# Performance work log

Measured on AMD Instinct MI355X. Metric: run time of the kernel, lower is better.

## Reference

```python
import jax, jax.numpy as jnp
import numpy as np

D_MODEL = 1024
NUM_HEADS = 16
D_K = D_MODEL // NUM_HEADS
NEG_INF = -1e9


def setup_inputs() -> dict:
    key = jax.random.key(0)
    ks = jax.random.split(key, 12)
    B, N_IMG, L_Q = 32, 576, 256
    img = jax.random.normal(ks[0], (B, N_IMG, D_MODEL), dtype=jnp.float32)
    que = jax.random.normal(ks[1], (B, L_Q, D_MODEL), dtype=jnp.float32)
    mask_img = jax.random.randint(ks[2], (B, N_IMG), 0, 2, dtype=jnp.int32)
    mask_que = jax.random.randint(ks[3], (B, L_Q), 0, 2, dtype=jnp.int32)
    s = 0.02  # init scale keeps scores in a sane range
    Wi = jax.random.normal(ks[4], (3, D_MODEL, D_MODEL), dtype=jnp.float32) * s
    bi = jax.random.normal(ks[5], (3, D_MODEL), dtype=jnp.float32) * s
    Wq = jax.random.normal(ks[6], (3, D_MODEL, D_MODEL), dtype=jnp.float32) * s
    bq = jax.random.normal(ks[7], (3, D_MODEL), dtype=jnp.float32) * s
    Wp = jax.random.normal(ks[8], (2, D_MODEL, D_MODEL), dtype=jnp.float32) * s
    bp = jax.random.normal(ks[9], (2, D_MODEL), dtype=jnp.float32) * s
    return {"img": img, "que": que, "Wi": Wi, "bi": bi, "Wq": Wq, "bq": bq,
            "Wp": Wp, "bp": bp, "mask_img": mask_img, "mask_que": mask_que}


def _proj_heads(x, W, b):
    # torch Linear: x @ W.T + b, then [B, L, H, d_k] -> [B, H, L, d_k]
    B, L, _ = x.shape
    out = jnp.einsum("bld,ed->ble", x, W) + b
    return out.reshape(B, L, NUM_HEADS, D_K).transpose(0, 2, 1, 3)


def _attention(q, k, v, mask_key):
    # q: [B,H,Lq,dk], k/v: [B,H,Lk,dk], mask_key: [B,Lk] (0 = masked)
    scores = jnp.einsum("bhqd,bhkd->bhqk", q, k) / jnp.sqrt(jnp.asarray(D_K, q.dtype))
    scores = jnp.where(mask_key[:, None, None, :] == 0, NEG_INF, scores)
    p = jax.nn.softmax(scores, axis=-1)
    attn = jnp.einsum("bhqk,bhkd->bhqd", p, v)
    B, H, Lq, dk = attn.shape
    return attn.transpose(0, 2, 1, 3).reshape(B, Lq, H * dk)


def reference(img, que, Wi, bi, Wq, bq, Wp, bp, mask_img, mask_que):
    iq = _proj_heads(img, Wi[0], bi[0])
    ik = _proj_heads(img, Wi[1], bi[1])
    iv = _proj_heads(img, Wi[2], bi[2])
    qq = _proj_heads(que, Wq[0], bq[0])
    qk = _proj_heads(que, Wq[1], bq[1])
    qv = _proj_heads(que, Wq[2], bq[2])
    q2i = _attention(iq, qk, qv, mask_que)  # [B, N_img, d_model]
    i2q = _attention(qq, ik, iv, mask_img)  # [B, L_q, d_model]
    out0 = jnp.einsum("bld,ed->ble", q2i, Wp[0]) + bp[0]
    out1 = jnp.einsum("bld,ed->ble", i2q, Wp[1]) + bp[1]
    return (out0, out1)
```

## Files before the change

kernel.cpp:

```cpp
#include <hip/hip_runtime.h>


typedef __bf16 bf16;
typedef __attribute__((ext_vector_type(8))) __bf16 bf16x8;
typedef __attribute__((ext_vector_type(4))) __bf16 bf16x4;
typedef __attribute__((ext_vector_type(2))) __bf16 bf16x2;
typedef __attribute__((ext_vector_type(4))) float f32x4;

__device__ __forceinline__ void g2lds16(const void* g, void* l) {
  __builtin_amdgcn_global_load_lds((const __attribute__((address_space(1))) void*)g,
                                   (__attribute__((address_space(3))) void*)l,
                                   16, 0, 0);
}

__global__ void cvt_bf16_multi(const float* s0, bf16* d0, int n0,
                               const float* s1, bf16* d1, int n1,
                               const float* s2, bf16* d2, int n2,
                               const float* s3, bf16* d3, int n3,
                               const float* s4, bf16* d4, int n4c) {
  const int total = n0 + n1 + n2 + n3 + n4c;
  const int stride = gridDim.x * blockDim.x;
  for (int i = blockIdx.x * blockDim.x + threadIdx.x; i < total; i += stride) {
    int j = i;
    const float* s; bf16* d;
    if (j < n0) { s = s0; d = d0; }
    else { j -= n0;
      if (j < n1) { s = s1; d = d1; }
      else { j -= n1;
        if (j < n2) { s = s2; d = d2; }
        else { j -= n2;
          if (j < n3) { s = s3; d = d3; }
          else { j -= n3; s = s4; d = d4; }
        }
      }
    }
    const float4 v = ((const float4*)s)[j];
    bf16x4 o = {(bf16)v.x, (bf16)v.y, (bf16)v.z, (bf16)v.w};
    ((bf16x4*)d)[j] = o;
  }
}

template <int MODE>
__global__ __launch_bounds__(512, 2)
void gemm_bt(const bf16* __restrict__ A, const bf16* __restrict__ Bw,
             const float* __restrict__ bias, void* __restrict__ outp, int Lrow) {
  __shared__ alignas(16) bf16 As[3][256 * 64];
  __shared__ alignas(16) bf16 Bs[3][128 * 64];
  const int tid = threadIdx.x;
  const int w = tid >> 6, lane = tid & 63;
  const int lr = lane & 15, quad = lane >> 4;
  const int i_q4 = quad * 4;
  const int mBase = blockIdx.y * 256, nBase = blockIdx.x * 128;
  const int wr = (w >> 1) * 64, wc = (w & 1) * 64;

  const int swl = (((lane & 7) ^ ((lane >> 3) & 7)) * 8);
  const bf16* Ab = A + (size_t)(mBase + (lane >> 3)) * 1024 + swl;
  const bf16* Bb = Bw + (size_t)(nBase + (lane >> 3)) * 1024 + swl;

  auto STAGE = [&](int kt, int s) {
    const int k0 = kt * 64;
#pragma unroll
    for (int c = 0; c < 4; ++c) {
      const int r = w * 32 + c * 8;
      g2lds16(Ab + (size_t)r * 1024 + k0, &As[s][r * 64]);
    }
#pragma unroll
    for (int c = 0; c < 2; ++c) {
      const int r = w * 16 + c * 8;
      g2lds16(Bb + (size_t)r * 1024 + k0, &Bs[s][r * 64]);
    }
  };

  f32x4 acc[4][4] = {};

  STAGE(0, 0);
  STAGE(1, 1);
  asm volatile("s_waitcnt vmcnt(6)" ::: "memory");
  __builtin_amdgcn_s_barrier();

  int s0 = 0;
  for (int t = 0; t < 16; ++t) {
    const int s2 = (s0 >= 1) ? s0 - 1 : s0 + 2;
    if (t + 2 < 16) STAGE(t + 2, s2);
    bf16x8 a[2][4], b[2][4];
#pragma unroll
    for (int ks = 0; ks < 2; ++ks) {
      const int sOff = ((quad | (ks << 2)) ^ (lr & 7)) * 8;
      const bf16* Ar = &As[s0][(wr + lr) * 64 + sOff];
      const bf16* Br = &Bs[s0][(wc + lr) * 64 + sOff];
#pragma unroll
      for (int i = 0; i < 4; ++i) a[ks][i] = *(const bf16x8*)(Ar + i * 1024);
#pragma unroll
      for (int j = 0; j < 4; ++j) b[ks][j] = *(const bf16x8*)(Br + j * 1024);
    }
    __builtin_amdgcn_s_setprio(1);
#pragma unroll
    for (int ks = 0; ks < 2; ++ks)
#pragma unroll
      for (int i = 0; i < 4; ++i)
#pragma unroll
        for (int j = 0; j < 4; ++j)
          acc[i][j] = __builtin_amdgcn_mfma_f32_16x16x32_bf16(a[ks][i], b[ks][j], acc[i][j], 0, 0, 0);
    __builtin_amdgcn_s_setprio(0);
    if (t < 14) {
      asm volatile("s_waitcnt vmcnt(6)" ::: "memory");
      __builtin_amdgcn_s_barrier();
    } else if (t == 14) {
      asm volatile("s_waitcnt vmcnt(0)" ::: "memory");
      __builtin_amdgcn_s_barrier();
    }
    s0 = (s0 < 2) ? s0 + 1 : 0;
  }

  if constexpr (MODE == 1) {
    float* out = (float*)outp;
#pragma unroll
    for (int j = 0; j < 4; ++j) {
      const int e = nBase + wc + j * 16 + lr;
      const float bv = bias[e];
#pragma unroll
      for (int i = 0; i < 4; ++i) {
        const int mb = mBase + wr + i * 16 + i_q4;
#pragma unroll
        for (int r = 0; r < 4; ++r)
          out[(size_t)(mb + r) * 1024 + e] = acc[i][j][r] + bv;
      }
    }
  } else {
    bf16* out = (bf16*)outp;
    const int L = Lrow;
    const size_t slab = (size_t)512 * L * 64;
    int bb[4], ll[4];
#pragma unroll
    for (int i = 0; i < 4; ++i) {
      const int m = mBase + wr + i * 16 + i_q4;
      bb[i] = m / L;
      ll[i] = m - bb[i] * L;
    }
#pragma unroll
    for (int j = 0; j < 4; ++j) {
      const int eb = nBase + wc + j * 16;
      const int p = eb >> 10, h = (eb >> 6) & 15, d = (eb & 63) + lr;
      const float bv = bias[eb + lr];
      if (p < 2) {
        bf16* o2 = out + (size_t)p * slab;
#pragma unroll
        for (int i = 0; i < 4; ++i) {
          bf16* o3 = o2 + ((size_t)(bb[i] * 16 + h) * L + ll[i]) * 64 + d;
#pragma unroll
          for (int r = 0; r < 4; ++r) o3[r * 64] = (bf16)(acc[i][j][r] + bv);
        }
      } else {
        bf16* o2 = out + 2 * slab;
#pragma unroll
        for (int i = 0; i < 4; ++i) {
          bf16x4 v;
#pragma unroll
          for (int r = 0; r < 4; ++r) v[r] = (bf16)(acc[i][j][r] + bv);
          *(bf16x4*)(o2 + ((size_t)(bb[i] * 16 + h) * 64 + d) * L + ll[i]) = v;
        }
      }
    }
  }
}

#define PSTR 40
__global__ __launch_bounds__(256)
void attn(const bf16* __restrict__ Q, const bf16* __restrict__ K,
          const bf16* __restrict__ Vt, const int* __restrict__ mask,
          bf16* __restrict__ out, int Lq, int Lk) {
  __shared__ float mk[576];
  __shared__ alignas(16) bf16 pb[4][2][2][16 * PSTR];
  const int tid = threadIdx.x;
  const int w = tid >> 6, lane = tid & 63;
  const int lr = lane & 15, quad = lane >> 4, i_q4 = quad * 4;
  const int bh = blockIdx.y, b = bh >> 4, h = bh & 15;
  const int q0 = blockIdx.x * 128 + w * 32;

  for (int k = tid; k < Lk; k += 256)
    mk[k] = (mask[b * Lk + k] == 0) ? -1e9f : 0.0f;
  __syncthreads();
  if (q0 >= Lq) return;

  bf16x8 qa[2][2];
#pragma unroll
  for (int i = 0; i < 2; ++i) {
    const bf16* Qb = Q + ((size_t)bh * Lq + q0 + i * 16 + lr) * 64 + quad * 8;
    qa[i][0] = *(const bf16x8*)(Qb);
    qa[i][1] = *(const bf16x8*)(Qb + 32);
  }
  const bf16* Kb = K + (size_t)bh * Lk * 64;
  const bf16* Vb = Vt + (size_t)bh * 64 * Lk;

  bf16x8 kc[2][2], kn[2][2], vc[4], vn[4];
  {
    const bf16* kp = Kb + (size_t)(lr * 2) * 64 + quad * 8;
    kc[0][0] = *(const bf16x8*)(kp);       kc[0][1] = *(const bf16x8*)(kp + 32);
    kc[1][0] = *(const bf16x8*)(kp + 64);  kc[1][1] = *(const bf16x8*)(kp + 96);
    const bf16* vp = Vb + quad * 8;
#pragma unroll
    for (int j = 0; j < 4; ++j) vc[j] = *(const bf16x8*)(vp + (size_t)(j * 16 + lr) * Lk);
  }

  f32x4 o[2][4] = {};
  float ls[2][4] = {};
  const int nkt = Lk >> 5;
  constexpr float SCL = 0.18033688f;
#pragma unroll 2
  for (int kt = 0; kt < nkt; ++kt) {
    const int kp1 = (kt + 1 < nkt) ? kt + 1 : kt;
    {
      const bf16* kp = Kb + ((size_t)kp1 * 32 + lr * 2) * 64 + quad * 8;
      kn[0][0] = *(const bf16x8*)(kp);       kn[0][1] = *(const bf16x8*)(kp + 32);
      kn[1][0] = *(const bf16x8*)(kp + 64);  kn[1][1] = *(const bf16x8*)(kp + 96);
      const bf16* vp = Vb + kp1 * 32 + quad * 8;
#pragma unroll
      for (int j = 0; j < 4; ++j) vn[j] = *(const bf16x8*)(vp + (size_t)(j * 16 + lr) * Lk);
    }

    f32x4 c[2][2];
#pragma unroll
    for (int i = 0; i < 2; ++i)
#pragma unroll
      for (int jn = 0; jn < 2; ++jn) {
        const f32x4 z = {};
        c[i][jn] = __builtin_amdgcn_mfma_f32_16x16x32_bf16(qa[i][0], kc[jn][0], z, 0, 0, 0);
        c[i][jn] = __builtin_amdgcn_mfma_f32_16x16x32_bf16(qa[i][1], kc[jn][1], c[i][jn], 0, 0, 0);
      }

    const float m0 = mk[kt * 32 + lr * 2], m1 = mk[kt * 32 + lr * 2 + 1];
#pragma unroll
    for (int i = 0; i < 2; ++i) {
      bf16* pw = &pb[w][kt & 1][i][0];
#pragma unroll
      for (int r = 0; r < 4; ++r) {
        const float p0 = __builtin_amdgcn_exp2f(__builtin_fmaf(c[i][0][r], SCL, m0));
        const float p1 = __builtin_amdgcn_exp2f(__builtin_fmaf(c[i][1][r], SCL, m1));
        ls[i][r] += p0 + p1;
        bf16x2 pp = {(bf16)p0, (bf16)p1};
        *(bf16x2*)(pw + (i_q4 + r) * PSTR + lr * 2) = pp;
      }
    }
#pragma unroll
    for (int i = 0; i < 2; ++i) {
      const bf16x8 pa = *(const bf16x8*)(&pb[w][kt & 1][i][0] + lr * PSTR + quad * 8);
#pragma unroll
      for (int j = 0; j < 4; ++j)
        o[i][j] = __builtin_amdgcn_mfma_f32_16x16x32_bf16(pa, vc[j], o[i][j], 0, 0, 0);
    }
#pragma unroll
    for (int jn = 0; jn < 2; ++jn)
#pragma unroll
      for (int kh = 0; kh < 2; ++kh) kc[jn][kh] = kn[jn][kh];
#pragma unroll
    for (int j = 0; j < 4; ++j) vc[j] = vn[j];
  }

  float inv[2][4];
#pragma unroll
  for (int i = 0; i < 2; ++i)
#pragma unroll
    for (int r = 0; r < 4; ++r) {
      float s = ls[i][r];
#pragma unroll
      for (int off = 1; off < 16; off <<= 1) s += __shfl_xor(s, off);
      inv[i][r] = 1.0f / s;
    }

#pragma unroll
  for (int i = 0; i < 2; ++i) {
    bf16* ob = out + ((size_t)b * Lq + q0 + i * 16 + i_q4) * 1024 + h * 64;
#pragma unroll
    for (int j = 0; j < 4; ++j)
#pragma unroll
      for (int r = 0; r < 4; ++r)
        ob[(size_t)r * 1024 + j * 16 + lr] = (bf16)(o[i][j][r] * inv[i][r]);
  }
}

extern "C" void kernel_launch(void* const* d_in, const int* in_sizes, int n_in,
                              void* d_out, int out_size, void* d_ws, size_t ws_size,
                              hipStream_t stream) {
  const float* img = (const float*)d_in[0];
  const float* que = (const float*)d_in[1];
  const float* Wi  = (const float*)d_in[2];
  const float* bi  = (const float*)d_in[3];
  const float* Wq  = (const float*)d_in[4];
  const float* bq  = (const float*)d_in[5];
  const float* Wp  = (const float*)d_in[6];
  const float* bp  = (const float*)d_in[7];
  const int* mimg = (const int*)d_in[8];
  const int* mque = (const int*)d_in[9];
  float* out = (float*)d_out;

  bf16* X1  = (bf16*)d_ws;
  bf16* X2  = X1 + 18874368;
  bf16* WiB = X2 + 8388608;
  bf16* WqB = WiB + 3145728;
  bf16* WpB = WqB + 3145728;
  bf16* PI  = WpB + 2097152;
  bf16* PQ  = PI + 56623104;

  cvt_bf16_multi<<<8192, 256, 0, stream>>>(img, X1, 18874368 / 4,
                                           que, X2, 8388608 / 4,
                                           Wi, WiB, 3145728 / 4,
                                           Wq, WqB, 3145728 / 4,
                                           Wp, WpB, 2097152 / 4);

  gemm_bt<0><<<dim3(24, 72), 512, 0, stream>>>(X1, WiB, bi, PI, 576);
  gemm_bt<0><<<dim3(24, 32), 512, 0, stream>>>(X2, WqB, bq, PQ, 256);

  const size_t SI = 18874368, SQ = 8388608;
  attn<<<dim3(5, 512), 256, 0, stream>>>(PI, PQ + SQ, PQ + 2 * SQ, mque, X1, 576, 256);
  attn<<<dim3(2, 512), 256, 0, stream>>>(PQ, PI + SI, PI + 2 * SI, mimg, X2, 256, 576);

  gemm_bt<1><<<dim3(8, 72), 512, 0, stream>>>(X1, WpB, bp, out, 0);
  gemm_bt<1><<<dim3(8, 32), 512, 0, stream>>>(X2, WpB + 1048576, bp + 1024, out + 18874368, 0);
}
```

Measured before the change: 753.7 us.

## Use 256x256 GEMM tiles with phased MFMA/LDS schedule and merge paired launches

The GEMM tile grows from 256x128 to 256x256 with 2-stage double buffering instead of 3. Each k-step is split into four MFMA quadrants, with LDS reads and global-to-LDS prefetches interleaved between barriers, and sched_barrier fences pin the ordering. The paired img/que projection GEMMs and the two attention directions are each merged into one launch that splits on a block index, which removes launch overhead and tail gaps. The larger tile doubles the accumulator registers (acc[8][4]) and adds many barriers, which could hurt occupancy or stall waves.

```diff
diff --git a/kernel.cpp b/kernel.cpp
--- a/kernel.cpp
+++ b/kernel.cpp
@@ -6,6 +6,9 @@
 typedef __attribute__((ext_vector_type(4))) __bf16 bf16x4;
 typedef __attribute__((ext_vector_type(2))) __bf16 bf16x2;
 typedef __attribute__((ext_vector_type(4))) float f32x4;
+
+#define SCHED0 __builtin_amdgcn_sched_barrier(0)
+#define BAR() do { SCHED0; __builtin_amdgcn_s_barrier(); SCHED0; } while (0)
 
 __device__ __forceinline__ void g2lds16(const void* g, void* l) {
   __builtin_amdgcn_global_load_lds((const __attribute__((address_space(1))) void*)g,
@@ -42,74 +45,137 @@
 
 template <int MODE>
 __global__ __launch_bounds__(512, 2)
-void gemm_bt(const bf16* __restrict__ A, const bf16* __restrict__ Bw,
-             const float* __restrict__ bias, void* __restrict__ outp, int Lrow) {
-  __shared__ alignas(16) bf16 As[3][256 * 64];
-  __shared__ alignas(16) bf16 Bs[3][128 * 64];
+void gemm_bt(const bf16* __restrict__ A0, const bf16* __restrict__ W0,
+             const float* __restrict__ bi0, void* __restrict__ o0, int L0,
+             const bf16* __restrict__ A1, const bf16* __restrict__ W1,
+             const float* __restrict__ bi1, void* __restrict__ o1, int L1,
+             int ySplit) {
+  __shared__ alignas(16) bf16 As[2][256 * 64];
+  __shared__ alignas(16) bf16 Bs[2][256 * 64];
   const int tid = threadIdx.x;
   const int w = tid >> 6, lane = tid & 63;
-  const int lr = lane & 15, quad = lane >> 4;
-  const int i_q4 = quad * 4;
-  const int mBase = blockIdx.y * 256, nBase = blockIdx.x * 128;
-  const int wr = (w >> 1) * 64, wc = (w & 1) * 64;
+  const int lr = lane & 15, quad = lane >> 4, i_q4 = quad * 4;
+  const int wm = w >> 2, wn = w & 3;
+  const int wr = wm * 128, wc = wn * 64;
+
+  const bf16* A; const bf16* Bw; const float* bias; void* outp; int Lrow;
+  int my = (int)blockIdx.y;
+  if (my < ySplit) { A = A0; Bw = W0; bias = bi0; outp = o0; Lrow = L0; }
+  else { my -= ySplit; A = A1; Bw = W1; bias = bi1; outp = o1; Lrow = L1; }
+  const int mBase = my * 256, nBase = (int)blockIdx.x * 256;
 
   const int swl = (((lane & 7) ^ ((lane >> 3) & 7)) * 8);
   const bf16* Ab = A + (size_t)(mBase + (lane >> 3)) * 1024 + swl;
   const bf16* Bb = Bw + (size_t)(nBase + (lane >> 3)) * 1024 + swl;
 
-  auto STAGE = [&](int kt, int s) {
-    const int k0 = kt * 64;
-#pragma unroll
-    for (int c = 0; c < 4; ++c) {
-      const int r = w * 32 + c * 8;
+  auto stA = [&](int kt, int half) {
+    const int s = kt & 1, k0 = kt * 64;
+#pragma unroll
+    for (int c = 0; c < 2; ++c) {
+      const int r = half * 128 + c * 64 + w * 8;
       g2lds16(Ab + (size_t)r * 1024 + k0, &As[s][r * 64]);
     }
+  };
+  auto stB = [&](int kt, int half) {
+    const int s = kt & 1, k0 = kt * 64;
 #pragma unroll
     for (int c = 0; c < 2; ++c) {
-      const int r = w * 16 + c * 8;
+      const int r = half * 128 + c * 64 + w * 8;
       g2lds16(Bb + (size_t)r * 1024 + k0, &Bs[s][r * 64]);
     }
   };
 
-  f32x4 acc[4][4] = {};
-
-  STAGE(0, 0);
-  STAGE(1, 1);
-  asm volatile("s_waitcnt vmcnt(6)" ::: "memory");
-  __builtin_amdgcn_s_barrier();
-
-  int s0 = 0;
+  f32x4 acc[8][4] = {};
+
+  stA(0, 0); stA(0, 1); stB(0, 0); stB(0, 1);
+  stA(1, 0); stA(1, 1); stB(1, 0); stB(1, 1);
+  asm volatile("s_waitcnt vmcnt(8)" ::: "memory");
+  BAR();
+
+  const int so0 = (quad ^ (lr & 7)) * 8;
+  const int so1 = ((quad | 4) ^ (lr & 7)) * 8;
+
+  bf16x8 a[8][2], b[4][2];
+#pragma unroll 2
   for (int t = 0; t < 16; ++t) {
-    const int s2 = (s0 >= 1) ? s0 - 1 : s0 + 2;
-    if (t + 2 < 16) STAGE(t + 2, s2);
-    bf16x8 a[2][4], b[2][4];
-#pragma unroll
-    for (int ks = 0; ks < 2; ++ks) {
-      const int sOff = ((quad | (ks << 2)) ^ (lr & 7)) * 8;
-      const bf16* Ar = &As[s0][(wr + lr) * 64 + sOff];
-      const bf16* Br = &Bs[s0][(wc + lr) * 64 + sOff];
-#pragma unroll
-      for (int i = 0; i < 4; ++i) a[ks][i] = *(const bf16x8*)(Ar + i * 1024);
-#pragma unroll
-      for (int j = 0; j < 4; ++j) b[ks][j] = *(const bf16x8*)(Br + j * 1024);
-    }
+    const bf16* Asb = As[t & 1];
+    const bf16* Bsb = Bs[t & 1];
+#pragma unroll
+    for (int i = 0; i < 4; ++i) {
+      const bf16* p = Asb + (wr + i * 16 + lr) * 64;
+      a[i][0] = *(const bf16x8*)(p + so0);
+      a[i][1] = *(const bf16x8*)(p + so1);
+    }
+#pragma unroll
+    for (int j = 0; j < 2; ++j) {
+      const bf16* p = Bsb + (wc + j * 16 + lr) * 64;
+      b[j][0] = *(const bf16x8*)(p + so0);
+      b[j][1] = *(const bf16x8*)(p + so1);
+    }
+    BAR();
     __builtin_amdgcn_s_setprio(1);
 #pragma unroll
     for (int ks = 0; ks < 2; ++ks)
 #pragma unroll
       for (int i = 0; i < 4; ++i)
 #pragma unroll
-        for (int j = 0; j < 4; ++j)
-          acc[i][j] = __builtin_amdgcn_mfma_f32_16x16x32_bf16(a[ks][i], b[ks][j], acc[i][j], 0, 0, 0);
+        for (int j = 0; j < 2; ++j)
+          acc[i][j] = __builtin_amdgcn_mfma_f32_16x16x32_bf16(a[i][ks], b[j][ks], acc[i][j], 0, 0, 0);
+    __builtin_amdgcn_s_setprio(0);
+    BAR();
+#pragma unroll
+    for (int i = 4; i < 8; ++i) {
+      const bf16* p = Asb + (wr + i * 16 + lr) * 64;
+      a[i][0] = *(const bf16x8*)(p + so0);
+      a[i][1] = *(const bf16x8*)(p + so1);
+    }
+    BAR();
+    __builtin_amdgcn_s_setprio(1);
+#pragma unroll
+    for (int ks = 0; ks < 2; ++ks)
+#pragma unroll
+      for (int i = 4; i < 8; ++i)
+#pragma unroll
+        for (int j = 0; j < 2; ++j)
+          acc[i][j] = __builtin_amdgcn_mfma_f32_16x16x32_bf16(a[i][ks], b[j][ks], acc[i][j], 0, 0, 0);
+    __builtin_amdgcn_s_setprio(0);
+    BAR();
+#pragma unroll
+    for (int j = 2; j < 4; ++j) {
+      const bf16* p = Bsb + (wc + j * 16 + lr) * 64;
+      b[j][0] = *(const bf16x8*)(p + so0);
+      b[j][1] = *(const bf16x8*)(p + so1);
+    }
+    if (t + 2 < 16) stA(t + 2, 0);
+    BAR();
+    __builtin_amdgcn_s_setprio(1);
+#pragma unroll
+    for (int ks = 0; ks < 2; ++ks)
+#pragma unroll
+      for (int i = 0; i < 4; ++i)
+#pragma unroll
+        for (int j = 2; j < 4; ++j)
+          acc[i][j] = __builtin_amdgcn_mfma_f32_16x16x32_bf16(a[i][ks], b[j][ks], acc[i][j], 0, 0, 0);
+    __builtin_amdgcn_s_setprio(0);
+    BAR();
+    if (t + 2 < 16) { stA(t + 2, 1); stB(t + 2, 0); stB(t + 2, 1); }
+    BAR();
+    __builtin_amdgcn_s_setprio(1);
+#pragma unroll
+    for (int ks = 0; ks < 2; ++ks)
+#pragma unroll
+      for (int i = 4; i < 8; ++i)
+#pragma unroll
+        for (int j = 2; j < 4; ++j)
+          acc[i][j] = __builtin_amdgcn_mfma_f32_16x16x32_bf16(a[i][ks], b[j][ks], acc[i][j], 0, 0, 0);
     __builtin_amdgcn_s_setprio(0);
     if (t < 14) {
-      asm volatile("s_waitcnt vmcnt(6)" ::: "memory");
-      __builtin_amdgcn_s_barrier();
+      asm volatile("s_waitcnt vmcnt(8)" ::: "memory");
+      BAR();
     } else if (t == 14) {
       asm volatile("s_waitcnt vmcnt(0)" ::: "memory");
-      __builtin_amdgcn_s_barrier();
-    }
-    s0 = (s0 < 2) ? s0 + 1 : 0;
+      BAR();
+    }
   }
 
   if constexpr (MODE == 1) {
@@ -119,7 +185,7 @@
       const int e = nBase + wc + j * 16 + lr;
       const float bv = bias[e];
 #pragma unroll
-      for (int i = 0; i < 4; ++i) {
+      for (int i = 0; i < 8; ++i) {
         const int mb = mBase + wr + i * 16 + i_q4;
 #pragma unroll
         for (int r = 0; r < 4; ++r)
@@ -130,9 +196,9 @@
     bf16* out = (bf16*)outp;
     const int L = Lrow;
     const size_t slab = (size_t)512 * L * 64;
-    int bb[4], ll[4];
-#pragma unroll
-    for (int i = 0; i < 4; ++i) {
+    int bb[8], ll[8];
+#pragma unroll
+    for (int i = 0; i < 8; ++i) {
       const int m = mBase + wr + i * 16 + i_q4;
       bb[i] = m / L;
       ll[i] = m - bb[i] * L;
@@ -145,7 +211,7 @@
       if (p < 2) {
         bf16* o2 = out + (size_t)p * slab;
 #pragma unroll
-        for (int i = 0; i < 4; ++i) {
+        for (int i = 0; i < 8; ++i) {
           bf16* o3 = o2 + ((size_t)(bb[i] * 16 + h) * L + ll[i]) * 64 + d;
 #pragma unroll
           for (int r = 0; r < 4; ++r) o3[r * 64] = (bf16)(acc[i][j][r] + bv);
@@ -153,7 +219,7 @@
       } else {
         bf16* o2 = out + 2 * slab;
 #pragma unroll
-        for (int i = 0; i < 4; ++i) {
+        for (int i = 0; i < 8; ++i) {
           bf16x4 v;
 #pragma unroll
           for (int r = 0; r < 4; ++r) v[r] = (bf16)(acc[i][j][r] + bv);
@@ -166,16 +232,24 @@
 
 #define PSTR 40
 __global__ __launch_bounds__(256)
-void attn(const bf16* __restrict__ Q, const bf16* __restrict__ K,
-          const bf16* __restrict__ Vt, const int* __restrict__ mask,
-          bf16* __restrict__ out, int Lq, int Lk) {
+void attn(const bf16* __restrict__ Q0, const bf16* __restrict__ K0,
+          const bf16* __restrict__ V0, const int* __restrict__ mk0,
+          bf16* __restrict__ ou0, int Lq0, int Lk0, int xSplit,
+          const bf16* __restrict__ Q1, const bf16* __restrict__ K1,
+          const bf16* __restrict__ V1, const int* __restrict__ mk1,
+          bf16* __restrict__ ou1, int Lq1, int Lk1) {
   __shared__ float mk[576];
   __shared__ alignas(16) bf16 pb[4][2][2][16 * PSTR];
   const int tid = threadIdx.x;
   const int w = tid >> 6, lane = tid & 63;
   const int lr = lane & 15, quad = lane >> 4, i_q4 = quad * 4;
   const int bh = blockIdx.y, b = bh >> 4, h = bh & 15;
-  const int q0 = blockIdx.x * 128 + w * 32;
+
+  const bf16* Q; const bf16* K; const bf16* Vt; const int* mask; bf16* out;
+  int Lq, Lk, gx = (int)blockIdx.x;
+  if (gx < xSplit) { Q = Q0; K = K0; Vt = V0; mask = mk0; out = ou0; Lq = Lq0; Lk = Lk0; }
+  else { gx -= xSplit; Q = Q1; K = K1; Vt = V1; mask = mk1; out = ou1; Lq = Lq1; Lk = Lk1; }
+  const int q0 = gx * 128 + w * 32;
 
   for (int k = tid; k < Lk; k += 256)
     mk[k] = (mask[b * Lk + k] == 0) ? -1e9f : 0.0f;
@@ -307,13 +381,13 @@
                                            Wq, WqB, 3145728 / 4,
                                            Wp, WpB, 2097152 / 4);
 
-  gemm_bt<0><<<dim3(24, 72), 512, 0, stream>>>(X1, WiB, bi, PI, 576);
-  gemm_bt<0><<<dim3(24, 32), 512, 0, stream>>>(X2, WqB, bq, PQ, 256);
+  gemm_bt<0><<<dim3(12, 104), 512, 0, stream>>>(X1, WiB, bi, PI, 576,
+                                                X2, WqB, bq, PQ, 256, 72);
 
   const size_t SI = 18874368, SQ = 8388608;
-  attn<<<dim3(5, 512), 256, 0, stream>>>(PI, PQ + SQ, PQ + 2 * SQ, mque, X1, 576, 256);
-  attn<<<dim3(2, 512), 256, 0, stream>>>(PQ, PI + SI, PI + 2 * SI, mimg, X2, 256, 576);
-
-  gemm_bt<1><<<dim3(8, 72), 512, 0, stream>>>(X1, WpB, bp, out, 0);
-  gemm_bt<1><<<dim3(8, 32), 512, 0, stream>>>(X2, WpB + 1048576, bp + 1024, out + 18874368, 0);
-}
+  attn<<<dim3(7, 512), 256, 0, stream>>>(PI, PQ + SQ, PQ + 2 * SQ, mque, X1, 576, 256, 5,
+                                         PQ, PI + SI, PI + 2 * SI, mimg, X2, 256, 576);
+
+  gemm_bt<1><<<dim3(4, 104), 512, 0, stream>>>(X1, WpB, bp, out, 0,
+                                               X2, WpB + 1048576, bp + 1024, out + 18874368, 0, 72);
+}
```

Result: faster. 663.7 us (-11.9%).
